# Kernel optimization log

Hardware: AMD Instinct MI355X
Metric: run time of the kernel (lower is better)

Reference implementation:

```python
import jax, jax.numpy as jnp
import numpy as np

B, S, D_IN, D_OUT, H = 4, 2048, 1024, 1024, 16
DH = D_OUT // H


def setup_inputs() -> dict:
    key = jax.random.key(0)
    k1, k2, k3 = jax.random.split(key, 3)
    payload = jax.random.normal(k1, (B, S, D_IN), dtype=jnp.float32)
    w_qkv = jax.random.normal(k2, (D_IN, 3 * D_OUT), dtype=jnp.float32) * (D_IN ** -0.5)
    w_out = jax.random.normal(k3, (D_OUT, D_OUT), dtype=jnp.float32) * (D_OUT ** -0.5)
    b_out = jnp.zeros((D_OUT,), dtype=jnp.float32)
    return {"payload": payload, "w_qkv": w_qkv, "w_out": w_out, "b_out": b_out}


def reference(payload, w_qkv, w_out, b_out):
    b, t, _ = payload.shape
    h, dh = H, DH
    qkv = payload @ w_qkv  # [b, t, 3*D_OUT]
    q, k, v = jnp.split(qkv, 3, axis=-1)
    # [b, t, h, dh] -> [b, h, t, dh]
    q = q.reshape(b, t, h, dh).transpose(0, 2, 1, 3)
    k = k.reshape(b, t, h, dh).transpose(0, 2, 1, 3)
    v = v.reshape(b, t, h, dh).transpose(0, 2, 1, 3)
    scores = jnp.einsum("bhqd,bhkd->bhqk", q, k) / jnp.sqrt(jnp.float32(dh))
    causal = jnp.tril(jnp.ones((t, t), dtype=bool))  # True = keep
    scores = jnp.where(causal, scores, -jnp.inf)
    weights = jax.nn.softmax(scores, axis=-1)
    # dropout_rate = 0.0 -> identity
    ctx = jnp.einsum("bhqk,bhkd->bhqd", weights, v)
    ctx = ctx.transpose(0, 2, 1, 3).reshape(b, t, h * dh)
    return ctx @ w_out + b_out
```

## Files before the change

kernel.cpp:

```cpp
#include <hip/hip_runtime.h>

#define NB 4
#define NS 2048
#define NH 16
#define NDH 64

typedef short bf16x8 __attribute__((ext_vector_type(8)));
typedef short bf16x4 __attribute__((ext_vector_type(4)));
typedef float f32x4 __attribute__((ext_vector_type(4)));
typedef unsigned short u16;
typedef unsigned int u32;

static __device__ __forceinline__ u16 f2bf(float f) {
  unsigned u = __float_as_uint(f);
  u += 0x7fffu + ((u >> 16) & 1u);
  return (u16)(u >> 16);
}

#define GLDS(gp, lp) __builtin_amdgcn_global_load_lds( \
    (const __attribute__((address_space(1))) void*)(gp), \
    (__attribute__((address_space(3))) void*)(lp), 16, 0, 0)

__global__ void cvt_k(const float* __restrict__ in, u16* __restrict__ out, int n) {
  int i = (blockIdx.x * 256 + threadIdx.x) * 8;
  if (i >= n) return;
  float4 a = *(const float4*)&in[i];
  float4 b = *(const float4*)&in[i + 4];
  bf16x8 u;
  u[0] = (short)f2bf(a.x); u[1] = (short)f2bf(a.y);
  u[2] = (short)f2bf(a.z); u[3] = (short)f2bf(a.w);
  u[4] = (short)f2bf(b.x); u[5] = (short)f2bf(b.y);
  u[6] = (short)f2bf(b.z); u[7] = (short)f2bf(b.w);
  *(bf16x8*)&out[i] = u;
}

__global__ void trcvt_k(const float* __restrict__ in, u16* __restrict__ out, int R, int C) {
  __shared__ float t[32][33];
  int c0 = blockIdx.x * 32, r0 = blockIdx.y * 32;
  int tx = threadIdx.x & 7, ty = threadIdx.x >> 3;
  float4 v = *(const float4*)&in[(size_t)(r0 + ty) * C + c0 + tx * 4];
  t[ty][tx * 4 + 0] = v.x; t[ty][tx * 4 + 1] = v.y;
  t[ty][tx * 4 + 2] = v.z; t[ty][tx * 4 + 3] = v.w;
  __syncthreads();
  ushort4 o;
  o.x = f2bf(t[tx * 4 + 0][ty]); o.y = f2bf(t[tx * 4 + 1][ty]);
  o.z = f2bf(t[tx * 4 + 2][ty]); o.w = f2bf(t[tx * 4 + 3][ty]);
  *(ushort4*)&out[(size_t)(c0 + ty) * R + r0 + tx * 4] = o;
}

template<int MODE>
__global__ __launch_bounds__(256)
void gemm_k(const u16* __restrict__ A, const u16* __restrict__ Bt,
            int M, int N, int K,
            u16* __restrict__ Qo, u16* __restrict__ Ko, u16* __restrict__ VTo,
            float* __restrict__ Co, const float* __restrict__ bias) {
  __shared__ __align__(16) u16 As[128 * 32];
  __shared__ __align__(16) u16 Bs[128 * 32];
  const int tid = threadIdx.x;
  const int w = tid >> 6, l = tid & 63;
  const int lr = l & 15, lg = l >> 4;
  const int wr = w >> 1, wc = w & 1;
  const int m0 = blockIdx.y * 128, n0 = blockIdx.x * 128;

  f32x4 acc[4][4] = {};

  const int srow = l >> 2;
  const int scol = (l & 3) * 8;
  const int nk = K >> 5;
  for (int kt = 0; kt < nk; ++kt) {
    __syncthreads();
    const int k0 = kt * 32;
#pragma unroll
    for (int c = 0; c < 2; ++c) {
      int chunk = w * 2 + c;
      int row = chunk * 16 + srow;
      GLDS(A  + (size_t)(m0 + row) * K + k0 + scol, As + chunk * 512);
      GLDS(Bt + (size_t)(n0 + row) * K + k0 + scol, Bs + chunk * 512);
    }
    __syncthreads();
    bf16x8 af[4];
#pragma unroll
    for (int mi = 0; mi < 4; ++mi)
      af[mi] = *(const bf16x8*)&As[(wr * 64 + mi * 16 + lr) * 32 + lg * 8];
#pragma unroll
    for (int ni = 0; ni < 4; ++ni) {
      bf16x8 bfr = *(const bf16x8*)&Bs[(wc * 64 + ni * 16 + lr) * 32 + lg * 8];
#pragma unroll
      for (int mi = 0; mi < 4; ++mi)
        acc[mi][ni] = __builtin_amdgcn_mfma_f32_16x16x32_bf16(af[mi], bfr, acc[mi][ni], 0, 0, 0);
    }
  }

#pragma unroll
  for (int mi = 0; mi < 4; ++mi) {
#pragma unroll
    for (int ni = 0; ni < 4; ++ni) {
#pragma unroll
      for (int r = 0; r < 4; ++r) {
        int gm = m0 + wr * 64 + mi * 16 + lg * 4 + r;
        int gn = n0 + wc * 64 + ni * 16 + lr;
        float v = acc[mi][ni][r];
        if (MODE == 0) {
          int which = gn >> 10, hd = gn & 1023;
          int b = gm >> 11, s = gm & 2047;
          int bh = b * NH + (hd >> 6), dh = hd & 63;
          if (which == 0)      Qo[((size_t)bh * NS + s) * NDH + dh] = f2bf(v * 0.1803368801111204f);
          else if (which == 1) Ko[((size_t)bh * NS + s) * NDH + dh] = f2bf(v);
          else                 VTo[((size_t)bh * NDH + dh) * NS + s] = f2bf(v);
        } else {
          Co[(size_t)gm * N + gn] = v + bias[gn];
        }
      }
    }
  }
}

__global__ __launch_bounds__(512)
void attn_k(const u16* __restrict__ Q, const u16* __restrict__ Kg,
            const u16* __restrict__ VTg, u16* __restrict__ CTX) {
  const int bh = blockIdx.x;
  const int pr = blockIdx.y;
  const int tid = threadIdx.x, w = tid >> 6, l = tid & 63;
  const int lr = l & 15, lg = l >> 4;
  const u16* Qh  = Q   + (size_t)bh * NS * NDH;
  const u16* Kh  = Kg  + (size_t)bh * NS * NDH;
  const u16* Vth = VTg + (size_t)bh * NDH * NS;

  __shared__ __align__(16) u16 Ks[2][64 * 64];
  __shared__ __align__(16) u16 Vs[2][64 * 64];

  const int srow_ = tid >> 3;
  const int colb  = (tid & 7) * 16;
  const int scolb = colb ^ ((srow_ & 7) << 4);
  const int kSrcOff = srow_ * NDH + (scolb >> 1);
  const int vSrcOff = srow_ * NS + (scolb >> 1);
  const int ldsOff  = w * 1024;

#define STAGE(t, buf) do {                                          \
    GLDS(Kh  + (size_t)(t) * 64 * NDH + kSrcOff, (char*)Ks[buf] + ldsOff); \
    GLDS(Vth + (size_t)(t) * 64       + vSrcOff, (char*)Vs[buf] + ldsOff); \
  } while (0)

  const int swz = (lr & 7) << 4;
  const int b = bh >> 4, h = bh & 15;

  for (int pass = 0; pass < 2; ++pass) {
    const int qt = pass == 0 ? pr : 15 - pr;

    const int qrow = qt * 128 + w * 16 + lr;
    bf16x8 qf[2];
    qf[0] = *(const bf16x8*)&Qh[(size_t)qrow * NDH + 0 * 32 + lg * 8];
    qf[1] = *(const bf16x8*)&Qh[(size_t)qrow * NDH + 1 * 32 + lg * 8];

    f32x4 o[4] = {};
    float lrun = 0.f;
    const int qmin = qt * 128 + w * 16;

    __syncthreads();
    STAGE(0, 0);
    __syncthreads();

    const int NT = 2 * qt + 2;
    for (int kt = 0; kt < NT; ++kt) {
      const int cur = kt & 1;
      if (kt + 1 < NT) STAGE(kt + 1, cur ^ 1);

      f32x4 sc[4] = {};
#pragma unroll
      for (int kk = 0; kk < 2; ++kk) {
#pragma unroll
        for (int kg = 0; kg < 4; ++kg) {
          bf16x8 kf = *(const bf16x8*)((const char*)Ks[cur] +
                       ((kg * 16 + lr) * 128 + ((kk * 64 + lg * 16) ^ swz)));
          sc[kg] = __builtin_amdgcn_mfma_f32_16x16x32_bf16(kf, qf[kk], sc[kg], 0, 0, 0);
        }
      }

      float sum = 0.f;
      if (kt * 64 + 63 > qmin) {
#pragma unroll
        for (int kg = 0; kg < 4; ++kg)
#pragma unroll
          for (int r = 0; r < 4; ++r) {
            int kglob = kt * 64 + kg * 16 + lg * 4 + r;
            float e = (kglob > qrow) ? 0.f : exp2f(sc[kg][r]);
            sc[kg][r] = e; sum += e;
          }
      } else {
#pragma unroll
        for (int kg = 0; kg < 4; ++kg)
#pragma unroll
          for (int r = 0; r < 4; ++r) {
            float e = exp2f(sc[kg][r]);
            sc[kg][r] = e; sum += e;
          }
      }
      lrun += sum;

#pragma unroll
      for (int half = 0; half < 2; ++half) {
        union { u32 wd[4]; bf16x8 v; } pk;
#pragma unroll
        for (int w2 = 0; w2 < 4; ++w2) {
          float lo = sc[half * 2 + (w2 >> 1)][2 * (w2 & 1)];
          float hi = sc[half * 2 + (w2 >> 1)][2 * (w2 & 1) + 1];
          asm("v_cvt_pk_bf16_f32 %0, %1, %2" : "=v"(pk.wd[w2]) : "v"(lo), "v"(hi));
        }
        bf16x8 pf = pk.v;
#pragma unroll
        for (int dhg = 0; dhg < 4; ++dhg) {
          const char* vrow = (const char*)Vs[cur] + (dhg * 16 + lr) * 128;
          bf16x4 va = *(const bf16x4*)(vrow + ((half * 64 + lg * 8) ^ swz));
          bf16x4 vb = *(const bf16x4*)(vrow + ((half * 64 + 32 + lg * 8) ^ swz));
          bf16x8 vf = __builtin_shufflevector(va, vb, 0, 1, 2, 3, 4, 5, 6, 7);
          o[dhg] = __builtin_amdgcn_mfma_f32_16x16x32_bf16(pf, vf, o[dhg], 0, 0, 0);
        }
      }

      __syncthreads();
    }

    lrun += __shfl_xor(lrun, 16);
    lrun += __shfl_xor(lrun, 32);
    float linv = 1.0f / lrun;
#pragma unroll
    for (int r = 0; r < 4; ++r) {
      float lq = __shfl(linv, (l & 48) | (lg * 4 + r));
      int srow = qt * 128 + w * 16 + lg * 4 + r;
      size_t base = ((size_t)(b * NS + srow)) * (NH * NDH) + h * NDH;
#pragma unroll
      for (int dhg = 0; dhg < 4; ++dhg)
        CTX[base + dhg * 16 + lr] = f2bf(o[dhg][r] * lq);
    }
  }
#undef STAGE
}

extern "C" void kernel_launch(void* const* d_in, const int* in_sizes, int n_in,
                              void* d_out, int out_size, void* d_ws, size_t ws_size,
                              hipStream_t stream) {
  const float* payload = (const float*)d_in[0];
  const float* w_qkv   = (const float*)d_in[1];
  const float* w_out   = (const float*)d_in[2];
  const float* b_out   = (const float*)d_in[3];
  float* out = (float*)d_out;

  char* ws = (char*)d_ws;
  size_t o0 = 0;
  u16* Xb    = (u16*)(ws + o0); o0 += (size_t)8192 * 1024 * 2;
  u16* Wqkvt = (u16*)(ws + o0); o0 += (size_t)3072 * 1024 * 2;
  u16* Woutt = (u16*)(ws + o0); o0 += (size_t)1024 * 1024 * 2;
  u16* Qb    = (u16*)(ws + o0); o0 += (size_t)64 * 2048 * 64 * 2;
  u16* Kb    = (u16*)(ws + o0); o0 += (size_t)64 * 2048 * 64 * 2;
  u16* VTb   = (u16*)(ws + o0); o0 += (size_t)64 * 64 * 2048 * 2;
  u16* CTX   = Xb;

  cvt_k<<<dim3(4096), dim3(256), 0, stream>>>(payload, Xb, 8192 * 1024);
  trcvt_k<<<dim3(96, 32), dim3(256), 0, stream>>>(w_qkv, Wqkvt, 1024, 3072);
  trcvt_k<<<dim3(32, 32), dim3(256), 0, stream>>>(w_out, Woutt, 1024, 1024);
  gemm_k<0><<<dim3(24, 64), dim3(256), 0, stream>>>(Xb, Wqkvt, 8192, 3072, 1024,
                                                    Qb, Kb, VTb, nullptr, nullptr);
  attn_k<<<dim3(64, 8), dim3(512), 0, stream>>>(Qb, Kb, VTb, CTX);
  gemm_k<1><<<dim3(8, 64), dim3(256), 0, stream>>>(CTX, Woutt, 8192, 1024, 1024,
                                                   nullptr, nullptr, nullptr, out, b_out);
}
```

Measured before the change: 214.0 us.

## Double-buffer GEMM LDS tiles and enlarge block to 256x128 with 512 threads

The projection GEMMs now use 512-thread blocks computing 256x128 output tiles, with two LDS buffers so the next K-slice's global-to-LDS load is issued before computing on the current one. This aims to overlap memory loads with MFMA work and halve the number of barriers per K step. Each wave keeps the same 64x64 accumulator footprint, while LDS use doubles and the grid shrinks by half in M, which may reduce wave-level parallelism. Waits on the asynchronous LDS loads rely on the barrier at the end of each iteration.

After: 217.6 us. Within noise of the previous version (+1.7%).

```diff
diff --git a/kernel.cpp b/kernel.cpp
--- a/kernel.cpp
+++ b/kernel.cpp
@@ -49,46 +49,57 @@
 }
 
 template<int MODE>
-__global__ __launch_bounds__(256)
+__global__ __launch_bounds__(512)
 void gemm_k(const u16* __restrict__ A, const u16* __restrict__ Bt,
             int M, int N, int K,
             u16* __restrict__ Qo, u16* __restrict__ Ko, u16* __restrict__ VTo,
             float* __restrict__ Co, const float* __restrict__ bias) {
-  __shared__ __align__(16) u16 As[128 * 32];
-  __shared__ __align__(16) u16 Bs[128 * 32];
+  __shared__ __align__(16) u16 As[2][256 * 32];
+  __shared__ __align__(16) u16 Bs[2][128 * 32];
   const int tid = threadIdx.x;
   const int w = tid >> 6, l = tid & 63;
   const int lr = l & 15, lg = l >> 4;
   const int wr = w >> 1, wc = w & 1;
-  const int m0 = blockIdx.y * 128, n0 = blockIdx.x * 128;
+  const int m0 = blockIdx.y * 256, n0 = blockIdx.x * 128;
 
   f32x4 acc[4][4] = {};
 
-  const int srow = l >> 2;
-  const int scol = (l & 3) * 8;
+  const int arow0 = tid >> 2;
+  const int arow1 = 128 + (tid >> 2);
+  const int brow  = tid >> 2;
+  const int scol  = (tid & 3) * 8;
+  const int abase0 = (w * 64) * 16;
+  const int abase1 = (512 + w * 64) * 16;
+  const int bbase  = (w * 64) * 16;
+
+#define STAGE(kt, buf) do {                                              \
+    const int k0_ = (kt) * 32;                                           \
+    GLDS(A  + (size_t)(m0 + arow0) * K + k0_ + scol, (char*)As[buf] + abase0); \
+    GLDS(A  + (size_t)(m0 + arow1) * K + k0_ + scol, (char*)As[buf] + abase1); \
+    GLDS(Bt + (size_t)(n0 + brow ) * K + k0_ + scol, (char*)Bs[buf] + bbase);  \
+  } while (0)
+
   const int nk = K >> 5;
+  STAGE(0, 0);
+  __syncthreads();
+
   for (int kt = 0; kt < nk; ++kt) {
-    __syncthreads();
-    const int k0 = kt * 32;
-#pragma unroll
-    for (int c = 0; c < 2; ++c) {
-      int chunk = w * 2 + c;
-      int row = chunk * 16 + srow;
-      GLDS(A  + (size_t)(m0 + row) * K + k0 + scol, As + chunk * 512);
-      GLDS(Bt + (size_t)(n0 + row) * K + k0 + scol, Bs + chunk * 512);
-    }
-    __syncthreads();
+    const int cur = kt & 1;
+    if (kt + 1 < nk) STAGE(kt + 1, cur ^ 1);
+
     bf16x8 af[4];
 #pragma unroll
     for (int mi = 0; mi < 4; ++mi)
-      af[mi] = *(const bf16x8*)&As[(wr * 64 + mi * 16 + lr) * 32 + lg * 8];
+      af[mi] = *(const bf16x8*)&As[cur][(wr * 64 + mi * 16 + lr) * 32 + lg * 8];
 #pragma unroll
     for (int ni = 0; ni < 4; ++ni) {
-      bf16x8 bfr = *(const bf16x8*)&Bs[(wc * 64 + ni * 16 + lr) * 32 + lg * 8];
+      bf16x8 bfr = *(const bf16x8*)&Bs[cur][(wc * 64 + ni * 16 + lr) * 32 + lg * 8];
 #pragma unroll
       for (int mi = 0; mi < 4; ++mi)
         acc[mi][ni] = __builtin_amdgcn_mfma_f32_16x16x32_bf16(af[mi], bfr, acc[mi][ni], 0, 0, 0);
     }
+
+    __syncthreads();
   }
 
 #pragma unroll
@@ -113,6 +124,7 @@
       }
     }
   }
+#undef STAGE
 }
 
 __global__ __launch_bounds__(512)
@@ -258,9 +270,9 @@
   cvt_k<<<dim3(4096), dim3(256), 0, stream>>>(payload, Xb, 8192 * 1024);
   trcvt_k<<<dim3(96, 32), dim3(256), 0, stream>>>(w_qkv, Wqkvt, 1024, 3072);
   trcvt_k<<<dim3(32, 32), dim3(256), 0, stream>>>(w_out, Woutt, 1024, 1024);
-  gemm_k<0><<<dim3(24, 64), dim3(256), 0, stream>>>(Xb, Wqkvt, 8192, 3072, 1024,
+  gemm_k<0><<<dim3(24, 32), dim3(512), 0, stream>>>(Xb, Wqkvt, 8192, 3072, 1024,
                                                     Qb, Kb, VTb, nullptr, nullptr);
   attn_k<<<dim3(64, 8), dim3(512), 0, stream>>>(Qb, Kb, VTb, CTX);
-  gemm_k<1><<<dim3(8, 64), dim3(256), 0, stream>>>(CTX, Woutt, 8192, 1024, 1024,
+  gemm_k<1><<<dim3(8, 32), dim3(512), 0, stream>>>(CTX, Woutt, 8192, 1024, 1024,
                                                    nullptr, nullptr, nullptr, out, b_out);
 }
```

## Widen GEMM K-tile to 64 with XOR-swizzled LDS and larger QKV block

Applied to the files above, without the earlier changes.

The projection GEMM now stages 64-wide K slices instead of 32, which halves the number of barrier pairs per K loop. Shared-memory rows are XOR-swizzled by row index so the 128-byte row reads avoid LDS bank conflicts. The QKV GEMM switches to 512-thread blocks covering 256 rows, reusing each B tile across more rows. The cost is more LDS per block, which may lower occupancy, and still no double buffering.

New measurement: 198.5 us. 1.08x faster.

```diff
diff --git a/kernel.cpp b/kernel.cpp
--- a/kernel.cpp
+++ b/kernel.cpp
@@ -48,46 +48,64 @@
   *(ushort4*)&out[(size_t)(c0 + ty) * R + r0 + tx * 4] = o;
 }
 
-template<int MODE>
-__global__ __launch_bounds__(256)
+template<int MODE, int WM>
+__global__ __launch_bounds__(WM * 128)
 void gemm_k(const u16* __restrict__ A, const u16* __restrict__ Bt,
             int M, int N, int K,
             u16* __restrict__ Qo, u16* __restrict__ Ko, u16* __restrict__ VTo,
             float* __restrict__ Co, const float* __restrict__ bias) {
-  __shared__ __align__(16) u16 As[128 * 32];
-  __shared__ __align__(16) u16 Bs[128 * 32];
+  constexpr int T  = WM * 128;
+  constexpr int BM = WM * 64;
+  constexpr int RA = 4;
+  constexpr int RB = 1024 / T;
+  __shared__ __align__(16) u16 As[BM * 64];
+  __shared__ __align__(16) u16 Bs[128 * 64];
   const int tid = threadIdx.x;
   const int w = tid >> 6, l = tid & 63;
   const int lr = l & 15, lg = l >> 4;
   const int wr = w >> 1, wc = w & 1;
-  const int m0 = blockIdx.y * 128, n0 = blockIdx.x * 128;
+  const int m0 = blockIdx.y * BM, n0 = blockIdx.x * 128;
+  const int swz = (lr & 7) << 4;
 
   f32x4 acc[4][4] = {};
 
-  const int srow = l >> 2;
-  const int scol = (l & 3) * 8;
-  const int nk = K >> 5;
+  const int nk = K >> 6;
   for (int kt = 0; kt < nk; ++kt) {
     __syncthreads();
-    const int k0 = kt * 32;
-#pragma unroll
-    for (int c = 0; c < 2; ++c) {
-      int chunk = w * 2 + c;
-      int row = chunk * 16 + srow;
-      GLDS(A  + (size_t)(m0 + row) * K + k0 + scol, As + chunk * 512);
-      GLDS(Bt + (size_t)(n0 + row) * K + k0 + scol, Bs + chunk * 512);
-    }
-    __syncthreads();
-    bf16x8 af[4];
-#pragma unroll
-    for (int mi = 0; mi < 4; ++mi)
-      af[mi] = *(const bf16x8*)&As[(wr * 64 + mi * 16 + lr) * 32 + lg * 8];
-#pragma unroll
-    for (int ni = 0; ni < 4; ++ni) {
-      bf16x8 bfr = *(const bf16x8*)&Bs[(wc * 64 + ni * 16 + lr) * 32 + lg * 8];
+    const int k0 = kt * 64;
+#pragma unroll
+    for (int r2 = 0; r2 < RA; ++r2) {
+      int c = r2 * T + tid;
+      int row = c >> 3;
+      int scolb = ((c & 7) * 16) ^ ((row & 7) << 4);
+      GLDS(A + (size_t)(m0 + row) * K + k0 + (scolb >> 1),
+           (char*)As + (size_t)r2 * T * 16 + w * 1024);
+    }
+#pragma unroll
+    for (int r2 = 0; r2 < RB; ++r2) {
+      int c = r2 * T + tid;
+      int row = c >> 3;
+      int scolb = ((c & 7) * 16) ^ ((row & 7) << 4);
+      GLDS(Bt + (size_t)(n0 + row) * K + k0 + (scolb >> 1),
+           (char*)Bs + (size_t)r2 * T * 16 + w * 1024);
+    }
+    __syncthreads();
+
+#pragma unroll
+    for (int kk = 0; kk < 2; ++kk) {
+      bf16x8 af[4];
 #pragma unroll
       for (int mi = 0; mi < 4; ++mi)
-        acc[mi][ni] = __builtin_amdgcn_mfma_f32_16x16x32_bf16(af[mi], bfr, acc[mi][ni], 0, 0, 0);
+        af[mi] = *(const bf16x8*)((const char*)As +
+                  ((wr * 64 + mi * 16 + lr) * 128 + ((kk * 64 + lg * 16) ^ swz)));
+#pragma unroll
+      for (int ni = 0; ni < 4; ++ni) {
+        bf16x8 bfr = *(const bf16x8*)((const char*)Bs +
+                  ((wc * 64 + ni * 16 + lr) * 128 + ((kk * 64 + lg * 16) ^ swz)));
+#pragma unroll
+        for (int mi = 0; mi < 4; ++mi)
+          acc[mi][ni] = __builtin_amdgcn_mfma_f32_16x16x32_bf16(af[mi], bfr, acc[mi][ni], 0, 0, 0);
+      }
     }
   }
 
@@ -258,9 +276,9 @@
   cvt_k<<<dim3(4096), dim3(256), 0, stream>>>(payload, Xb, 8192 * 1024);
   trcvt_k<<<dim3(96, 32), dim3(256), 0, stream>>>(w_qkv, Wqkvt, 1024, 3072);
   trcvt_k<<<dim3(32, 32), dim3(256), 0, stream>>>(w_out, Woutt, 1024, 1024);
-  gemm_k<0><<<dim3(24, 64), dim3(256), 0, stream>>>(Xb, Wqkvt, 8192, 3072, 1024,
-                                                    Qb, Kb, VTb, nullptr, nullptr);
+  gemm_k<0, 4><<<dim3(24, 32), dim3(512), 0, stream>>>(Xb, Wqkvt, 8192, 3072, 1024,
+                                                       Qb, Kb, VTb, nullptr, nullptr);
   attn_k<<<dim3(64, 8), dim3(512), 0, stream>>>(Qb, Kb, VTb, CTX);
-  gemm_k<1><<<dim3(8, 64), dim3(256), 0, stream>>>(CTX, Woutt, 8192, 1024, 1024,
-                                                   nullptr, nullptr, nullptr, out, b_out);
-}
+  gemm_k<1, 2><<<dim3(8, 64), dim3(256), 0, stream>>>(CTX, Woutt, 8192, 1024, 1024,
+                                                      nullptr, nullptr, nullptr, out, b_out);
+}
```

## Triple-buffer GEMM loads with swizzled LDS and larger QKV tile

Applied to the files above, without the earlier changes.

Rewrites the bf16 GEMM main loop into a three-stage pipeline. Loads for tile t+2 are issued while tile t computes, with explicit vmcnt waits and raw barriers instead of two syncthreads per step. The LDS layout is XOR-swizzled to reduce bank conflicts on fragment reads, and MFMA issue is wrapped in setprio. The QKV projection moves to 256x128 tiles with 512 threads. This targets global-load latency and LDS conflicts, at the cost of more LDS per block and hand-tuned wait counts that must match the issued load count.

Result: faster. 208.3 us (-2.7%).

```diff
diff --git a/kernel.cpp b/kernel.cpp
--- a/kernel.cpp
+++ b/kernel.cpp
@@ -20,6 +20,10 @@
 #define GLDS(gp, lp) __builtin_amdgcn_global_load_lds( \
     (const __attribute__((address_space(1))) void*)(gp), \
     (__attribute__((address_space(3))) void*)(lp), 16, 0, 0)
+
+#define BAR   do { __builtin_amdgcn_s_barrier(); __builtin_amdgcn_sched_barrier(0); } while (0)
+#define VMC(n) do { asm volatile("s_waitcnt vmcnt(" #n ")" ::: "memory"); \
+                    __builtin_amdgcn_sched_barrier(0); } while (0)
 
 __global__ void cvt_k(const float* __restrict__ in, u16* __restrict__ out, int n) {
   int i = (blockIdx.x * 256 + threadIdx.x) * 8;
@@ -48,47 +52,81 @@
   *(ushort4*)&out[(size_t)(c0 + ty) * R + r0 + tx * 4] = o;
 }
 
-template<int MODE>
-__global__ __launch_bounds__(256)
+template<int MODE, int WM>
+__global__ __launch_bounds__(WM * 128)
 void gemm_k(const u16* __restrict__ A, const u16* __restrict__ Bt,
-            int M, int N, int K,
+            int K, int N,
             u16* __restrict__ Qo, u16* __restrict__ Ko, u16* __restrict__ VTo,
             float* __restrict__ Co, const float* __restrict__ bias) {
-  __shared__ __align__(16) u16 As[128 * 32];
-  __shared__ __align__(16) u16 Bs[128 * 32];
+  constexpr int T  = WM * 128;
+  constexpr int BM = WM * 64;
+  constexpr int RB = 512 / T;
+  constexpr int LPT = 2 + RB;
+  __shared__ __align__(16) u16 As[3][BM * 32];
+  __shared__ __align__(16) u16 Bs[3][128 * 32];
   const int tid = threadIdx.x;
   const int w = tid >> 6, l = tid & 63;
   const int lr = l & 15, lg = l >> 4;
   const int wr = w >> 1, wc = w & 1;
-  const int m0 = blockIdx.y * 128, n0 = blockIdx.x * 128;
+  const int m0 = blockIdx.y * BM, n0 = blockIdx.x * 128;
 
   f32x4 acc[4][4] = {};
 
-  const int srow = l >> 2;
-  const int scol = (l & 3) * 8;
+  const int sb = ((tid & 3) * 16) ^ (((tid >> 2) & 3) << 4);
+  const int srcA0 = (tid >> 2) * K + (sb >> 1);
+  const int srcA1 = (T / 4 + (tid >> 2)) * K + (sb >> 1);
+  int srcB[RB], dstB[RB];
+#pragma unroll
+  for (int r = 0; r < RB; ++r) {
+    srcB[r] = (r * (T / 4) + (tid >> 2)) * K + (sb >> 1);
+    dstB[r] = r * T * 16 + w * 1024;
+  }
+  const int dstA0 = w * 1024, dstA1 = T * 16 + w * 1024;
+
+#define STG(t, buf) do {                                              \
+    const u16* Ab_ = A  + (size_t)m0 * K + (t) * 32;                  \
+    const u16* Bb_ = Bt + (size_t)n0 * K + (t) * 32;                  \
+    GLDS(Ab_ + srcA0, (char*)As[buf] + dstA0);                        \
+    GLDS(Ab_ + srcA1, (char*)As[buf] + dstA1);                        \
+    _Pragma("unroll")                                                 \
+    for (int r = 0; r < RB; ++r)                                      \
+      GLDS(Bb_ + srcB[r], (char*)Bs[buf] + dstB[r]);                  \
+  } while (0)
+
+  const int rswz = (lr & 3) << 4;
   const int nk = K >> 5;
-  for (int kt = 0; kt < nk; ++kt) {
-    __syncthreads();
-    const int k0 = kt * 32;
-#pragma unroll
-    for (int c = 0; c < 2; ++c) {
-      int chunk = w * 2 + c;
-      int row = chunk * 16 + srow;
-      GLDS(A  + (size_t)(m0 + row) * K + k0 + scol, As + chunk * 512);
-      GLDS(Bt + (size_t)(n0 + row) * K + k0 + scol, Bs + chunk * 512);
+
+  STG(0, 0);
+  STG(1, 1);
+  if constexpr (WM == 4) { VMC(3); } else { VMC(4); }
+  BAR;
+
+  for (int t = 0; t < nk; ++t) {
+    const int cur = t % 3;
+    const char* Ar = (const char*)As[cur];
+    const char* Br = (const char*)Bs[cur];
+    bf16x8 af[4], bfr[4];
+#pragma unroll
+    for (int mi = 0; mi < 4; ++mi)
+      af[mi] = *(const bf16x8*)(Ar + (wr * 64 + mi * 16 + lr) * 64 + ((lg * 16) ^ rswz));
+#pragma unroll
+    for (int ni = 0; ni < 4; ++ni)
+      bfr[ni] = *(const bf16x8*)(Br + (wc * 64 + ni * 16 + lr) * 64 + ((lg * 16) ^ rswz));
+    if (t + 2 < nk) STG(t + 2, (t + 2) % 3);
+    BAR;
+    __builtin_amdgcn_s_setprio(1);
+#pragma unroll
+    for (int ni = 0; ni < 4; ++ni)
+#pragma unroll
+      for (int mi = 0; mi < 4; ++mi)
+        acc[mi][ni] = __builtin_amdgcn_mfma_f32_16x16x32_bf16(af[mi], bfr[ni], acc[mi][ni], 0, 0, 0);
+    __builtin_amdgcn_s_setprio(0);
+    if (t + 2 < nk) {
+      if constexpr (WM == 4) { VMC(3); } else { VMC(4); }
+    } else {
+      VMC(0);
     }
-    __syncthreads();
-    bf16x8 af[4];
-#pragma unroll
-    for (int mi = 0; mi < 4; ++mi)
-      af[mi] = *(const bf16x8*)&As[(wr * 64 + mi * 16 + lr) * 32 + lg * 8];
-#pragma unroll
-    for (int ni = 0; ni < 4; ++ni) {
-      bf16x8 bfr = *(const bf16x8*)&Bs[(wc * 64 + ni * 16 + lr) * 32 + lg * 8];
-#pragma unroll
-      for (int mi = 0; mi < 4; ++mi)
-        acc[mi][ni] = __builtin_amdgcn_mfma_f32_16x16x32_bf16(af[mi], bfr, acc[mi][ni], 0, 0, 0);
-    }
+    BAR;
   }
 
 #pragma unroll
@@ -113,6 +151,7 @@
       }
     }
   }
+#undef STG
 }
 
 __global__ __launch_bounds__(512)
@@ -258,9 +297,9 @@
   cvt_k<<<dim3(4096), dim3(256), 0, stream>>>(payload, Xb, 8192 * 1024);
   trcvt_k<<<dim3(96, 32), dim3(256), 0, stream>>>(w_qkv, Wqkvt, 1024, 3072);
   trcvt_k<<<dim3(32, 32), dim3(256), 0, stream>>>(w_out, Woutt, 1024, 1024);
-  gemm_k<0><<<dim3(24, 64), dim3(256), 0, stream>>>(Xb, Wqkvt, 8192, 3072, 1024,
-                                                    Qb, Kb, VTb, nullptr, nullptr);
+  gemm_k<0, 4><<<dim3(24, 32), dim3(512), 0, stream>>>(Xb, Wqkvt, 1024, 3072,
+                                                       Qb, Kb, VTb, nullptr, nullptr);
   attn_k<<<dim3(64, 8), dim3(512), 0, stream>>>(Qb, Kb, VTb, CTX);
-  gemm_k<1><<<dim3(8, 64), dim3(256), 0, stream>>>(CTX, Woutt, 8192, 1024, 1024,
-                                                   nullptr, nullptr, nullptr, out, b_out);
-}
+  gemm_k<1, 2><<<dim3(8, 64), dim3(256), 0, stream>>>(CTX, Woutt, 1024, 1024,
+                                                      nullptr, nullptr, nullptr, out, b_out);
+}
```
